# Optimization experiments

Measured on AMD Instinct MI355X. Metric: run time of the kernel, lower is better.

The kernel has to match this reference:

```python
import jax, jax.numpy as jnp
import numpy as np

N, E1, E2, P, H = 4096, 131072, 131072, 65536, 128
ROLE_VOCAB, ROLE_DIM, IDX_VOCAB, IDX_DIM = 8, 16, 1024, 8


def _lin_init(key, fan_in, fan_out):
    k1, k2 = jax.random.split(key)
    bound = 1.0 / np.sqrt(fan_in)
    W = jax.random.uniform(k1, (fan_in, fan_out), jnp.float32, -bound, bound)
    b = jax.random.uniform(k2, (fan_out,), jnp.float32, -bound, bound)
    return W, b


def setup_inputs() -> dict:
    key = jax.random.key(0)
    ks = jax.random.split(key, 24)
    d = {}
    d["block_features"] = jax.random.normal(ks[0], (N, 16), jnp.float32)
    d["role_ids"] = jax.random.randint(ks[1], (N,), 0, ROLE_VOCAB)
    d["b2b_src"] = jax.random.randint(ks[2], (E1,), 0, N)
    d["b2b_dst"] = jax.random.randint(ks[3], (E1,), 0, N)
    d["b2b_w"] = jax.random.uniform(ks[4], (E1,), jnp.float32)
    d["p2b_pin"] = jax.random.randint(ks[5], (E2,), 0, P)
    d["p2b_block"] = jax.random.randint(ks[6], (E2,), 0, N)
    d["p2b_w"] = jax.random.uniform(ks[7], (E2,), jnp.float32)
    d["pins_pos"] = jax.random.normal(ks[8], (P, 2), jnp.float32)
    d["area_targets"] = jax.random.uniform(ks[9], (N,), jnp.float32)
    # parameters
    d["role_emb"] = jax.random.normal(ks[10], (ROLE_VOCAB, ROLE_DIM), jnp.float32)
    d["idx_emb"] = jax.random.normal(ks[11], (IDX_VOCAB, IDX_DIM), jnp.float32)
    d["in_W1"], d["in_b1"] = _lin_init(ks[12], 16 + IDX_DIM + ROLE_DIM, H)
    d["in_W2"], d["in_b2"] = _lin_init(ks[13], H, H)
    d["b2b_W1"], d["b2b_b1"] = _lin_init(ks[14], 2 * H + 1, H)
    d["b2b_W2"], d["b2b_b2"] = _lin_init(ks[15], H, H)
    d["p2b_W1"], d["p2b_b1"] = _lin_init(ks[16], H + 3, H)
    d["p2b_W2"], d["p2b_b2"] = _lin_init(ks[17], H, H)
    d["self_W"], d["self_b"] = _lin_init(ks[18], H, H)
    d["ln_g"] = jnp.ones((H,), jnp.float32)
    d["ln_b"] = jnp.zeros((H,), jnp.float32)
    d["gp_W1"], d["gp_b1"] = _lin_init(ks[19], 2 * H, H)
    d["gp_W2"], d["gp_b2"] = _lin_init(ks[20], H, H)
    return d


def _mlp2(x, W1, b1, W2, b2):
    return jax.nn.relu(x @ W1 + b1) @ W2 + b2


def _forward(block_features, role_ids, b2b_src, b2b_dst, b2b_w, p2b_pin, p2b_block,
             p2b_w, pins_pos, area_targets, role_emb, idx_emb, in_W1, in_b1, in_W2,
             in_b2, b2b_W1, b2b_b1, b2b_W2, b2b_b2, p2b_W1, p2b_b1, p2b_W2, p2b_b2,
             self_W, self_b, ln_g, ln_b, gp_W1, gp_b1, gp_W2, gp_b2):
    n = block_features.shape[0]
    role_e = role_emb[role_ids]                       # [N, role_dim]
    idx_e = idx_emb[jnp.arange(n) % IDX_VOCAB]        # [N, idx_dim]
    x = jnp.concatenate([block_features, role_e, idx_e], axis=-1)
    h = jax.nn.relu(_mlp2(x, in_W1, in_b1, in_W2, in_b2))  # input_proj ends in ReLU

    # --- b2b messages: two directed messages per undirected edge ---
    max_b2b = jax.lax.stop_gradient(jnp.maximum(jnp.max(jnp.abs(b2b_w)), 1.0))
    w = (b2b_w / max_b2b)[:, None]                    # [E1, 1]
    hi, hj = h[b2b_src], h[b2b_dst]                   # [E1, H]
    m_ij = _mlp2(jnp.concatenate([hi, hj, w], -1), b2b_W1, b2b_b1, b2b_W2, b2b_b2)
    m_ji = _mlp2(jnp.concatenate([hj, hi, w], -1), b2b_W1, b2b_b1, b2b_W2, b2b_b2)
    agg = jnp.zeros_like(h).at[b2b_src].add(m_ij).at[b2b_dst].add(m_ji)

    # --- p2b messages ---
    total_area = jnp.maximum(jnp.sum(area_targets), 1e-6)
    case_scale = jax.lax.stop_gradient(jnp.maximum(jnp.sqrt(total_area), 1e-6))
    max_p2b = jax.lax.stop_gradient(jnp.maximum(jnp.max(jnp.abs(p2b_w)), 1.0))
    pin_feats = jnp.concatenate(
        [pins_pos[p2b_pin] / case_scale, (p2b_w / max_p2b)[:, None]], axis=-1)  # [E2, 3]
    m_p = _mlp2(jnp.concatenate([h[p2b_block], pin_feats], -1),
                p2b_W1, p2b_b1, p2b_W2, p2b_b2)
    agg = agg.at[p2b_block].add(m_p)

    # --- combine + LayerNorm ---
    z = h @ self_W + self_b + agg
    mu = jnp.mean(z, axis=-1, keepdims=True)
    var = jnp.mean(jnp.square(z - mu), axis=-1, keepdims=True)
    block_embeddings = (z - mu) / jnp.sqrt(var + 1e-5) * ln_g + ln_b

    pooled = jnp.concatenate(
        [block_embeddings.mean(axis=0), block_embeddings.max(axis=0)], axis=-1)
    graph_embedding = _mlp2(pooled, gp_W1, gp_b1, gp_W2, gp_b2)
    return block_embeddings, graph_embedding


def reference(block_features, role_ids, b2b_src, b2b_dst, b2b_w, p2b_pin, p2b_block,
              p2b_w, pins_pos, area_targets, role_emb, idx_emb, in_W1, in_b1, in_W2,
              in_b2, b2b_W1, b2b_b1, b2b_W2, b2b_b2, p2b_W1, p2b_b1, p2b_W2, p2b_b2,
              self_W, self_b, ln_g, ln_b, gp_W1, gp_b1, gp_W2, gp_b2):
    block_embeddings, graph_embedding = _forward(
        block_features, role_ids, b2b_src, b2b_dst, b2b_w, p2b_pin, p2b_block,
        p2b_w, pins_pos, area_targets, role_emb, idx_emb, in_W1, in_b1, in_W2,
        in_b2, b2b_W1, b2b_b1, b2b_W2, b2b_b2, p2b_W1, p2b_b1, p2b_W2, p2b_b2,
        self_W, self_b, ln_g, ln_b, gp_W1, gp_b1, gp_W2, gp_b2)
    block_mask = jnp.ones((block_features.shape[0],), dtype=bool)
    return block_embeddings, graph_embedding, block_mask
```

## Files before the change

### kernel.cpp

```cpp
#include <hip/hip_runtime.h>
#include <hip/hip_bf16.h>

#define N_NODES 4096
#define HDIM    128
#define E1      131072
#define E2      131072
#define NMSG_B2B (2 * E1)
#define CAPB    192
#define CAPP    96

#define OFF_PSUM   8
#define OFF_PMAX   136
#define OFF_HB     264
#define OFF_P      (OFF_HB + 262144)
#define OFF_Q      (OFF_P + 524288)
#define OFF_R      (OFF_Q + 524288)
#define OFF_CP     (OFF_R + 524288)
#define OFF_B2H    (OFF_CP + 24576)
#define OFF_B2L    (OFF_B2H + 8192)
#define OFF_P2H    (OFF_B2L + 8192)
#define OFF_P2L    (OFF_P2H + 8192)
#define OFF_SWP    (OFF_P2L + 8192)
#define OFF_IW1    (OFF_SWP + 8192)
#define OFF_IW2    (OFF_IW1 + 4096)
#define OFF_WLAST  (OFF_IW2 + 8192)
#define OFF_PEXTRA (OFF_WLAST + 128)
#define OFF_CNTB   (OFF_PEXTRA + 384)
#define OFF_CNTP   (OFF_CNTB + 4096)
#define OFF_BKB    (OFF_CNTP + 4096)
#define OFF_BKP    (OFF_BKB + 2 * N_NODES * CAPB)
#define WS_FLOATS  (OFF_BKP + 2 * N_NODES * CAPP)

typedef short short8 __attribute__((ext_vector_type(8)));
typedef float f32x4 __attribute__((ext_vector_type(4)));

__device__ __forceinline__ unsigned short f2bf(float f) {
  union { float f; unsigned u; } v; v.f = f;
  unsigned r = v.u + 0x7fffu + ((v.u >> 16) & 1u);
  return (unsigned short)(r >> 16);
}
__device__ __forceinline__ float bf2f(unsigned short h) {
  return __uint_as_float((unsigned)h << 16);
}
__device__ __forceinline__ int il(int c) { return ((c & 63) << 1) | (c >> 6); }

__global__ __launch_bounds__(256) void setup_kernel(const float* __restrict__ b2bw,
                                                    const float* __restrict__ p2bw,
                                                    const float* __restrict__ area,
                                                    const float* __restrict__ bW1,
                                                    const float* __restrict__ bW2,
                                                    const float* __restrict__ pW1,
                                                    const float* __restrict__ pW2,
                                                    const float* __restrict__ sWm,
                                                    const float* __restrict__ iW1,
                                                    const float* __restrict__ iW2,
                                                    float* __restrict__ ws) {
  __shared__ float red[256];
  int b = blockIdx.x, t = threadIdx.x;
  if (b < 32) {
    float m = 0.f;
    for (int i = b * 256 + t; i < E1; i += 32 * 256) m = fmaxf(m, fabsf(b2bw[i]));
    red[t] = m; __syncthreads();
    for (int s = 128; s > 0; s >>= 1) { if (t < s) red[t] = fmaxf(red[t], red[t + s]); __syncthreads(); }
    if (t == 0) atomicMax((unsigned*)&ws[0], __float_as_uint(red[0]));
  } else if (b < 64) {
    float m = 0.f;
    for (int i = (b - 32) * 256 + t; i < E2; i += 32 * 256) m = fmaxf(m, fabsf(p2bw[i]));
    red[t] = m; __syncthreads();
    for (int s = 128; s > 0; s >>= 1) { if (t < s) red[t] = fmaxf(red[t], red[t + s]); __syncthreads(); }
    if (t == 0) atomicMax((unsigned*)&ws[1], __float_as_uint(red[0]));
  } else if (b < 96) {
    float s0 = 0.f;
    for (int i = (b - 64) * 256 + t; i < N_NODES; i += 32 * 256) s0 += area[i];
    red[t] = s0; __syncthreads();
    for (int s = 128; s > 0; s >>= 1) { if (t < s) red[t] += red[t + s]; __syncthreads(); }
    if (t == 0) atomicAdd(&ws[2], red[0]);
  } else if (b == 96) {
    if (t < HDIM) ((int*)ws)[OFF_PMAX + t] = 0x80000000;
  } else {
    unsigned short* Cp  = (unsigned short*)(ws + OFF_CP);
    unsigned short* B2h = (unsigned short*)(ws + OFF_B2H);
    unsigned short* B2l = (unsigned short*)(ws + OFF_B2L);
    unsigned short* P2h = (unsigned short*)(ws + OFF_P2H);
    unsigned short* P2l = (unsigned short*)(ws + OFF_P2L);
    unsigned short* Swp = (unsigned short*)(ws + OFF_SWP);
    unsigned short* I1p = (unsigned short*)(ws + OFF_IW1);
    unsigned short* I2p = (unsigned short*)(ws + OFF_IW2);
    float* wlast = ws + OFF_WLAST;
    float* pextra = ws + OFF_PEXTRA;
    const int total = 156160;
    for (int x = (b - 97) * 256 + t; x < total; x += 128 * 256) {
      if (x < 49152) {
        int j = x & 7, lane = (x >> 3) & 63, ks = (x >> 9) & 3, nc = x >> 11;
        int col = nc * 16 + (lane & 15), k = ks * 32 + (lane >> 4) * 8 + j;
        float v;
        if (col < 128)      v = bW1[k * 128 + col];
        else if (col < 256) v = bW1[(128 + k) * 128 + (col - 128)];
        else                v = pW1[k * 128 + (col - 256)];
        Cp[x] = f2bf(v);
      } else if (x < 114688) {
        int u = (x - 49152) & 16383, which = (x - 49152) >> 14;
        int j = u & 7, lane = (u >> 3) & 63, ks = (u >> 9) & 3, nt = u >> 11;
        int n = nt * 16 + (lane & 15), k = ks * 32 + (lane >> 4) * 8 + j;
        float v = (which < 2) ? bW2[k * 128 + n] : pW2[k * 128 + n];
        unsigned short hi = f2bf(v);
        unsigned short outv = (which & 1) ? f2bf(v - bf2f(hi)) : hi;
        ((which < 2) ? ((which & 1) ? B2l : B2h) : ((which & 1) ? P2l : P2h))[u] = outv;
      } else if (x < 131072) {
        int u = x - 114688;
        int j = u & 7, lane = (u >> 3) & 63, ks = (u >> 9) & 3, nt = u >> 11;
        int n = nt * 16 + (lane & 15), k = ks * 32 + (lane >> 4) * 8 + j;
        Swp[u] = f2bf(sWm[k * 128 + n]);
      } else if (x < 139264) {
        int u = x - 131072;
        int j = u & 7, lane = (u >> 3) & 63, ks = (u >> 9) & 1, nt = u >> 10;
        int n = nt * 16 + (lane & 15), k = ks * 32 + (lane >> 4) * 8 + j;
        I1p[u] = (k < 40) ? f2bf(iW1[k * 128 + n]) : 0;
      } else if (x < 155648) {
        int u = x - 139264;
        int j = u & 7, lane = (u >> 3) & 63, ks = (u >> 9) & 3, nt = u >> 11;
        int n = nt * 16 + (lane & 15), k = ks * 32 + (lane >> 4) * 8 + j;
        I2p[u] = f2bf(iW2[k * 128 + n]);
      } else if (x < 155776) {
        int c = x - 155648;
        wlast[il(c)] = bW1[256 * 128 + c];
      } else {
        int u = x - 155776;
        int r = u >> 7, c = u & 127;
        pextra[r * 128 + il(c)] = pW1[(128 + r) * 128 + c];
      }
    }
  }
}

__global__ __launch_bounds__(512) void mid_kernel(const int* __restrict__ src,
                                                  const int* __restrict__ dst,
                                                  const int* __restrict__ pblk,
                                                  const int* __restrict__ ppin,
                                                  const float* __restrict__ bwv,
                                                  const float* __restrict__ pwv,
                                                  const float* __restrict__ pins,
                                                  const float* __restrict__ bfeat,
                                                  const int* __restrict__ rid,
                                                  const float* __restrict__ remb,
                                                  const float* __restrict__ iemb,
                                                  const float* __restrict__ ib1,
                                                  const float* __restrict__ ib2,
                                                  const float* __restrict__ bb1,
                                                  const float* __restrict__ pb1,
                                                  float* __restrict__ ws,
                                                  unsigned short* __restrict__ hb) {
  __shared__ __attribute__((aligned(16))) unsigned short xs[16 * 72];
  __shared__ __attribute__((aligned(16))) unsigned short h1s[16 * 136];
  __shared__ __attribute__((aligned(16))) unsigned short hs[16 * 136];
  int tid = threadIdx.x;
  if (blockIdx.x < 768) {
    int i = blockIdx.x * 512 + tid;
    int* cntB = (int*)ws + OFF_CNTB;
    int* cntP = (int*)ws + OFF_CNTP;
    uint2* BKB = (uint2*)((int*)ws + OFF_BKB);
    uint2* BKP = (uint2*)((int*)ws + OFF_BKP);
    if (i < NMSG_B2B) {
      int e = i >> 1, d = i & 1;
      int tg = d ? dst[e] : src[e];
      int o  = d ? src[e] : dst[e];
      int pos = atomicAdd(&cntB[tg], 1);
      if (pos < CAPB) {
        uint2 v; v.x = (unsigned)o; v.y = __float_as_uint(bwv[e]);
        BKB[tg * CAPB + pos] = v;
      }
    } else {
      int e = i - NMSG_B2B;
      int pin = ppin[e];
      int tg = pblk[e];
      int pos = atomicAdd(&cntP[tg], 1);
      if (pos < CAPP) {
        uint2 v;
        v.x = ((unsigned)f2bf(pins[pin * 2 + 1]) << 16) | (unsigned)f2bf(pins[pin * 2]);
        v.y = __float_as_uint(pwv[e]);
        BKP[tg * CAPP + pos] = v;
      }
    }
    return;
  }
  const unsigned short* I1p = (const unsigned short*)(ws + OFF_IW1);
  const unsigned short* I2p = (const unsigned short*)(ws + OFF_IW2);
  const unsigned short* Cp  = (const unsigned short*)(ws + OFF_CP);
  float* P = ws + OFF_P;
  float* Q = ws + OFF_Q;
  float* R = ws + OFF_R;
  int n0 = (blockIdx.x - 768) * 16;
  for (int idx = tid; idx < 1024; idx += 512) {
    int m = idx >> 6, c = idx & 63;
    int n = n0 + m;
    float v = 0.f;
    if (c < 16)      v = bfeat[n * 16 + c];
    else if (c < 32) v = remb[rid[n] * 16 + (c - 16)];
    else if (c < 40) v = iemb[(n & 1023) * 8 + (c - 32)];
    xs[m * 72 + c] = f2bf(v);
  }
  __syncthreads();
  int lane = tid & 63, wv = tid >> 6;
  int l15 = lane & 15, q = lane >> 4;
  f32x4 zero = {0.f, 0.f, 0.f, 0.f};
  f32x4 a1 = zero;
#pragma unroll
  for (int ks = 0; ks < 2; ks++) {
    short8 af = *(const short8*)(&xs[l15 * 72 + ks * 32 + q * 8]);
    short8 bfr = *(const short8*)(I1p + ((wv * 2 + ks) * 64 + lane) * 8);
    a1 = __builtin_amdgcn_mfma_f32_16x16x32_bf16(af, bfr, a1, 0, 0, 0);
  }
  {
    int n = wv * 16 + l15;
    float b = ib1[n];
#pragma unroll
    for (int r = 0; r < 4; r++)
      h1s[(q * 4 + r) * 136 + n] = f2bf(fmaxf(a1[r] + b, 0.f));
  }
  __syncthreads();
  f32x4 a2 = zero;
#pragma unroll
  for (int ks = 0; ks < 4; ks++) {
    short8 af = *(const short8*)(&h1s[l15 * 136 + ks * 32 + q * 8]);
    short8 bfr = *(const short8*)(I2p + ((wv * 4 + ks) * 64 + lane) * 8);
    a2 = __builtin_amdgcn_mfma_f32_16x16x32_bf16(af, bfr, a2, 0, 0, 0);
  }
  {
    int n = wv * 16 + l15;
    float b = ib2[n];
#pragma unroll
    for (int r = 0; r < 4; r++) {
      unsigned short hv = f2bf(fmaxf(a2[r] + b, 0.f));
      hs[(q * 4 + r) * 136 + n] = hv;
      hb[(n0 + q * 4 + r) * 128 + n] = hv;
    }
  }
  __syncthreads();
  f32x4 a3[3];
#pragma unroll
  for (int i = 0; i < 3; i++) a3[i] = zero;
#pragma unroll
  for (int ks = 0; ks < 4; ks++) {
    short8 af = *(const short8*)(&hs[l15 * 136 + ks * 32 + q * 8]);
#pragma unroll
    for (int j = 0; j < 3; j++) {
      short8 bfr = *(const short8*)(Cp + (((3 * wv + j) * 4 + ks) * 64 + lane) * 8);
      a3[j] = __builtin_amdgcn_mfma_f32_16x16x32_bf16(af, bfr, a3[j], 0, 0, 0);
    }
  }
#pragma unroll
  for (int j = 0; j < 3; j++) {
    int col = (3 * wv + j) * 16 + l15;
    int arr = col >> 7, cc = col & 127;
    float bias = (arr == 0) ? bb1[cc] : ((arr == 2) ? pb1[cc] : 0.f);
    float* dstp = (arr == 0) ? P : ((arr == 1) ? Q : R);
    int ic = il(cc);
#pragma unroll
    for (int r = 0; r < 4; r++)
      dstp[(n0 + q * 4 + r) * 128 + ic] = a3[j][r] + bias;
  }
}

__global__ __launch_bounds__(1024) void fused_kernel(const unsigned short* __restrict__ hb,
                                                     const float* __restrict__ sb,
                                                     const float* __restrict__ lng,
                                                     const float* __restrict__ lnb,
                                                     const float* __restrict__ bb2,
                                                     const float* __restrict__ pb2,
                                                     const float* __restrict__ gW1,
                                                     const float* __restrict__ gb1,
                                                     const float* __restrict__ gW2,
                                                     const float* __restrict__ gb2,
                                                     float* __restrict__ ws,
                                                     float* __restrict__ out) {
  __shared__ __attribute__((aligned(16))) unsigned short A[16 * 648];
  __shared__ float zp[2][16 * 128];
  __shared__ float zs[16 * 133];
  __shared__ float muS[16], rsg[16];
  __shared__ float partS[16][16], partQ[16][16];
  __shared__ float psumL[8][128];
  __shared__ int   pmaxL[8][128];
  __shared__ int   isLast;
  int tid = threadIdx.x;
  int n0 = blockIdx.x * 16;
  int lane = tid & 63, wv = tid >> 6;
  if (tid < 256) {
    int m = tid >> 4, o = (tid & 15) * 8;
    *(uint4*)(&A[m * 648 + o]) = *(const uint4*)(hb + (n0 + m) * 128 + o);
  }
  {
    const int* cntB = (const int*)ws + OFF_CNTB;
    const int* cntP = (const int*)ws + OFF_CNTP;
    const uint2* BKB = (const uint2*)((const int*)ws + OFF_BKB);
    const uint2* BKP = (const uint2*)((const int*)ws + OFF_BKP);
    const float* Pm = ws + OFF_P;
    const float* Qm = ws + OFF_Q;
    const float* Rm = ws + OFF_R;
    float invb = 1.f / fmaxf(__uint_as_float(((const unsigned*)ws)[0]), 1.f);
    float invp = 1.f / fmaxf(__uint_as_float(((const unsigned*)ws)[1]), 1.f);
    float cs = fmaxf(sqrtf(fmaxf(ws[2], 1e-6f)), 1e-6f);
    float invc = 1.f / cs;
    float2 wlr = *(const float2*)(ws + OFF_WLAST + 2 * lane);
    float2 e0r = *(const float2*)(ws + OFF_PEXTRA + 2 * lane);
    float2 e1r = *(const float2*)(ws + OFF_PEXTRA + 128 + 2 * lane);
    float2 e2r = *(const float2*)(ws + OFF_PEXTRA + 256 + 2 * lane);
    float2 wl = {invb * wlr.x, invb * wlr.y};
    float2 e0 = {invc * e0r.x, invc * e0r.y};
    float2 e1 = {invc * e1r.x, invc * e1r.y};
    float2 e2 = {invp * e2r.x, invp * e2r.y};
    int ln = wv;
    int node = n0 + ln;
    {
      int cnt = min(cntB[node], CAPB);
      const uint2* bk = BKB + node * CAPB;
      float2 p = *(const float2*)(Pm + node * 128 + 2 * lane);
      float a0 = 0.f, a1 = 0.f, b0 = 0.f, b1 = 0.f;
      int m = 0;
      for (; m + 8 <= cnt; m += 8) {
        uint2 k0 = bk[m],     k1 = bk[m + 1], k2 = bk[m + 2], k3 = bk[m + 3];
        uint2 k4 = bk[m + 4], k5 = bk[m + 5], k6 = bk[m + 6], k7 = bk[m + 7];
        float2 q0 = *(const float2*)(Qm + k0.x * 128 + 2 * lane);
        float2 q1 = *(const float2*)(Qm + k1.x * 128 + 2 * lane);
        float2 q2 = *(const float2*)(Qm + k2.x * 128 + 2 * lane);
        float2 q3 = *(const float2*)(Qm + k3.x * 128 + 2 * lane);
        float2 q4 = *(const float2*)(Qm + k4.x * 128 + 2 * lane);
        float2 q5 = *(const float2*)(Qm + k5.x * 128 + 2 * lane);
        float2 q6 = *(const float2*)(Qm + k6.x * 128 + 2 * lane);
        float2 q7 = *(const float2*)(Qm + k7.x * 128 + 2 * lane);
        float w0 = __uint_as_float(k0.y), w1 = __uint_as_float(k1.y);
        float w2 = __uint_as_float(k2.y), w3 = __uint_as_float(k3.y);
        float w4 = __uint_as_float(k4.y), w5 = __uint_as_float(k5.y);
        float w6 = __uint_as_float(k6.y), w7 = __uint_as_float(k7.y);
        a0 += fmaxf(fmaf(w0, wl.x, p.x) + q0.x, 0.f);
        a1 += fmaxf(fmaf(w0, wl.y, p.y) + q0.y, 0.f);
        b0 += fmaxf(fmaf(w1, wl.x, p.x) + q1.x, 0.f);
        b1 += fmaxf(fmaf(w1, wl.y, p.y) + q1.y, 0.f);
        a0 += fmaxf(fmaf(w2, wl.x, p.x) + q2.x, 0.f);
        a1 += fmaxf(fmaf(w2, wl.y, p.y) + q2.y, 0.f);
        b0 += fmaxf(fmaf(w3, wl.x, p.x) + q3.x, 0.f);
        b1 += fmaxf(fmaf(w3, wl.y, p.y) + q3.y, 0.f);
        a0 += fmaxf(fmaf(w4, wl.x, p.x) + q4.x, 0.f);
        a1 += fmaxf(fmaf(w4, wl.y, p.y) + q4.y, 0.f);
        b0 += fmaxf(fmaf(w5, wl.x, p.x) + q5.x, 0.f);
        b1 += fmaxf(fmaf(w5, wl.y, p.y) + q5.y, 0.f);
        a0 += fmaxf(fmaf(w6, wl.x, p.x) + q6.x, 0.f);
        a1 += fmaxf(fmaf(w6, wl.y, p.y) + q6.y, 0.f);
        b0 += fmaxf(fmaf(w7, wl.x, p.x) + q7.x, 0.f);
        b1 += fmaxf(fmaf(w7, wl.y, p.y) + q7.y, 0.f);
      }
      for (; m < cnt; m++) {
        uint2 k0 = bk[m];
        float w0 = __uint_as_float(k0.y);
        float2 q0 = *(const float2*)(Qm + k0.x * 128 + 2 * lane);
        a0 += fmaxf(fmaf(w0, wl.x, p.x) + q0.x, 0.f);
        a1 += fmaxf(fmaf(w0, wl.y, p.y) + q0.y, 0.f);
      }
      float s0 = a0 + b0;
      float s1 = a1 + b1;
      unsigned short h0 = f2bf(s0);
      A[ln * 648 + 128 + lane] = h0;
      A[ln * 648 + 256 + lane] = f2bf(s0 - bf2f(h0));
      unsigned short h1v = f2bf(s1);
      A[ln * 648 + 128 + 64 + lane] = h1v;
      A[ln * 648 + 256 + 64 + lane] = f2bf(s1 - bf2f(h1v));
    }
    {
      int cnt = min(cntP[node], CAPP);
      const uint2* bk = BKP + node * CAPP;
      float2 r = *(const float2*)(Rm + node * 128 + 2 * lane);
      float a0 = 0.f, a1 = 0.f, b0 = 0.f, b1 = 0.f;
      int m = 0;
      for (; m + 4 <= cnt; m += 4) {
        uint2 k0 = bk[m], k1 = bk[m + 1], k2 = bk[m + 2], k3 = bk[m + 3];
        float x00 = __uint_as_float((k0.x & 0xFFFFu) << 16);
        float x01 = __uint_as_float(k0.x & 0xFFFF0000u);
        float x02 = __uint_as_float(k0.y);
        float x10 = __uint_as_float((k1.x & 0xFFFFu) << 16);
        float x11 = __uint_as_float(k1.x & 0xFFFF0000u);
        float x12 = __uint_as_float(k1.y);
        float x20 = __uint_as_float((k2.x & 0xFFFFu) << 16);
        float x21 = __uint_as_float(k2.x & 0xFFFF0000u);
        float x22 = __uint_as_float(k2.y);
        float x30 = __uint_as_float((k3.x & 0xFFFFu) << 16);
        float x31 = __uint_as_float(k3.x & 0xFFFF0000u);
        float x32 = __uint_as_float(k3.y);
        a0 += fmaxf(fmaf(x02, e2.x, fmaf(x01, e1.x, fmaf(x00, e0.x, r.x))), 0.f);
        a1 += fmaxf(fmaf(x02, e2.y, fmaf(x01, e1.y, fmaf(x00, e0.y, r.y))), 0.f);
        b0 += fmaxf(fmaf(x12, e2.x, fmaf(x11, e1.x, fmaf(x10, e0.x, r.x))), 0.f);
        b1 += fmaxf(fmaf(x12, e2.y, fmaf(x11, e1.y, fmaf(x10, e0.y, r.y))), 0.f);
        a0 += fmaxf(fmaf(x22, e2.x, fmaf(x21, e1.x, fmaf(x20, e0.x, r.x))), 0.f);
        a1 += fmaxf(fmaf(x22, e2.y, fmaf(x21, e1.y, fmaf(x20, e0.y, r.y))), 0.f);
        b0 += fmaxf(fmaf(x32, e2.x, fmaf(x31, e1.x, fmaf(x30, e0.x, r.x))), 0.f);
        b1 += fmaxf(fmaf(x32, e2.y, fmaf(x31, e1.y, fmaf(x30, e0.y, r.y))), 0.f);
      }
      for (; m < cnt; m++) {
        uint2 k0 = bk[m];
        float x00 = __uint_as_float((k0.x & 0xFFFFu) << 16);
        float x01 = __uint_as_float(k0.x & 0xFFFF0000u);
        float x02 = __uint_as_float(k0.y);
        a0 += fmaxf(fmaf(x02, e2.x, fmaf(x01, e1.x, fmaf(x00, e0.x, r.x))), 0.f);
        a1 += fmaxf(fmaf(x02, e2.y, fmaf(x01, e1.y, fmaf(x00, e0.y, r.y))), 0.f);
      }
      float s0 = a0 + b0;
      float s1 = a1 + b1;
      unsigned short h0 = f2bf(s0);
      A[ln * 648 + 384 + lane] = h0;
      A[ln * 648 + 512 + lane] = f2bf(s0 - bf2f(h0));
      unsigned short h1v = f2bf(s1);
      A[ln * 648 + 384 + 64 + lane] = h1v;
      A[ln * 648 + 512 + 64 + lane] = f2bf(s1 - bf2f(h1v));
    }
  }
  __syncthreads();
  int l15 = lane & 15, q = lane >> 4;
  int ct = wv & 7, half = wv >> 3;
  f32x4 zero = {0.f, 0.f, 0.f, 0.f};
  f32x4 acc = zero;
  const unsigned short* bufs[7] = {
    (const unsigned short*)(ws + OFF_SWP), (const unsigned short*)(ws + OFF_B2H),
    (const unsigned short*)(ws + OFF_B2L), (const unsigned short*)(ws + OFF_B2H),
    (const unsigned short*)(ws + OFF_P2H), (const unsigned short*)(ws + OFF_P2L),
    (const unsigned short*)(ws + OFF_P2H)};
  const int segs[7] = {0, 128, 128, 256, 384, 384, 512};
  int p0 = half ? 4 : 0, p1 = half ? 7 : 4;
  for (int p = p0; p < p1; p++) {
#pragma unroll
    for (int ks = 0; ks < 4; ks++) {
      short8 af = *(const short8*)(&A[l15 * 648 + segs[p] + ks * 32 + q * 8]);
      short8 bfr = *(const short8*)(bufs[p] + ((ct * 4 + ks) * 64 + lane) * 8);
      acc = __builtin_amdgcn_mfma_f32_16x16x32_bf16(af, bfr, acc, 0, 0, 0);
    }
  }
  {
    int nn = ct * 16 + l15;
#pragma unroll
    for (int r = 0; r < 4; r++)
      zp[half][(q * 4 + r) * 128 + nn] = acc[r];
  }
  __syncthreads();
  const int* cntB = (const int*)ws + OFF_CNTB;
  const int* cntP = (const int*)ws + OFF_CNTP;
  {
    int idx = tid;
    for (int rep = 0; rep < 2; rep++, idx += 1024) {
      int row = idx >> 7, c = idx & 127;
      float cb = (float)cntB[n0 + row], cp = (float)cntP[n0 + row];
      zs[row * 133 + c] = zp[0][row * 128 + c] + zp[1][row * 128 + c]
                        + sb[c] + cb * bb2[c] + cp * pb2[c];
    }
  }
  __syncthreads();
  if (tid < 256) {
    int r = tid >> 4, g = tid & 15;
    const float* zr = &zs[r * 133 + g * 8];
    float s = 0.f, s2 = 0.f;
#pragma unroll
    for (int i = 0; i < 8; i++) { float v = zr[i]; s += v; s2 += v * v; }
    partS[r][g] = s; partQ[r][g] = s2;
  }
  __syncthreads();
  if (tid < 16) {
    float s = 0.f, s2 = 0.f;
#pragma unroll
    for (int g = 0; g < 16; g++) { s += partS[tid][g]; s2 += partQ[tid][g]; }
    float m = s * (1.f / 128.f);
    float var = s2 * (1.f / 128.f) - m * m;
    muS[tid] = m;
    rsg[tid] = rsqrtf(fmaxf(var, 0.f) + 1e-5f);
  }
  __syncthreads();
  {
    int c = tid & 127, grp = tid >> 7;
    float g = lng[c], b = lnb[c];
    float ls = 0.f; int lm = 0x80000000;
    for (int r = grp * 2; r < grp * 2 + 2; r++) {
      float v = (zs[r * 133 + c] - muS[r]) * rsg[r] * g + b;
      out[(n0 + r) * 128 + c] = v;
      ls += v;
      int e = __float_as_int(v);
      e = e >= 0 ? e : (e ^ 0x7fffffff);
      lm = max(lm, e);
    }
    psumL[grp][c] = ls; pmaxL[grp][c] = lm;
  }
  __syncthreads();
  if (tid < 128) {
    float s = 0.f; int mx = 0x80000000;
#pragma unroll
    for (int g = 0; g < 8; g++) { s += psumL[g][tid]; mx = max(mx, pmaxL[g][tid]); }
    atomicAdd(&ws[OFF_PSUM + tid], s);
    atomicMax(&((int*)ws)[OFF_PMAX + tid], mx);
  }
  if (tid < 16) out[N_NODES * HDIM + HDIM + n0 + tid] = 1.0f;
  __syncthreads();
  if (tid == 0) {
    __threadfence();
    int v = atomicAdd(&((int*)ws)[3], 1);
    isLast = (v == (int)gridDim.x - 1);
  }
  __syncthreads();
  if (!isLast) return;
  __shared__ float pooled[256];
  __shared__ float gpart[8][128];
  __shared__ float g1[128];
  if (tid < 128) {
    pooled[tid] = atomicAdd(&ws[OFF_PSUM + tid], 0.f) * (1.f / (float)N_NODES);
  } else if (tid < 256) {
    int e = atomicAdd(&((int*)ws)[OFF_PMAX + (tid - 128)], 0);
    int bits = e >= 0 ? e : (e ^ 0x7fffffff);
    pooled[tid] = __int_as_float(bits);
  }
  __syncthreads();
  {
    int c = tid & 127, g = tid >> 7;
    float acc2 = 0.f;
#pragma unroll 8
    for (int k = g * 32; k < g * 32 + 32; k++) acc2 += pooled[k] * gW1[k * 128 + c];
    gpart[g][c] = acc2;
  }
  __syncthreads();
  if (tid < 128) {
    float s = gb1[tid];
#pragma unroll
    for (int g = 0; g < 8; g++) s += gpart[g][tid];
    g1[tid] = fmaxf(s, 0.f);
  }
  __syncthreads();
  {
    int c = tid & 127, g = tid >> 7;
    float acc2 = 0.f;
#pragma unroll 8
    for (int k = g * 16; k < g * 16 + 16; k++) acc2 += g1[k] * gW2[k * 128 + c];
    gpart[g][c] = acc2;
  }
  __syncthreads();
  if (tid < 128) {
    float s = gb2[tid];
#pragma unroll
    for (int g = 0; g < 8; g++) s += gpart[g][tid];
    out[N_NODES * HDIM + tid] = s;
  }
}

extern "C" void kernel_launch(void* const* d_in, const int* in_sizes, int n_in,
                              void* d_out, int out_size, void* d_ws, size_t ws_size,
                              hipStream_t stream) {
  const float* bfeat = (const float*)d_in[0];
  const int*   rid   = (const int*)d_in[1];
  const int*   bsrc  = (const int*)d_in[2];
  const int*   bdst  = (const int*)d_in[3];
  const float* bw    = (const float*)d_in[4];
  const int*   ppin  = (const int*)d_in[5];
  const int*   pblk  = (const int*)d_in[6];
  const float* pw    = (const float*)d_in[7];
  const float* pins  = (const float*)d_in[8];
  const float* area  = (const float*)d_in[9];
  const float* remb  = (const float*)d_in[10];
  const float* iemb  = (const float*)d_in[11];
  const float* inW1  = (const float*)d_in[12];
  const float* inb1  = (const float*)d_in[13];
  const float* inW2  = (const float*)d_in[14];
  const float* inb2  = (const float*)d_in[15];
  const float* bW1   = (const float*)d_in[16];
  const float* bb1   = (const float*)d_in[17];
  const float* bW2   = (const float*)d_in[18];
  const float* bb2   = (const float*)d_in[19];
  const float* pW1   = (const float*)d_in[20];
  const float* pb1   = (const float*)d_in[21];
  const float* pW2   = (const float*)d_in[22];
  const float* pb2   = (const float*)d_in[23];
  const float* sW    = (const float*)d_in[24];
  const float* sb    = (const float*)d_in[25];
  const float* lng   = (const float*)d_in[26];
  const float* lnb   = (const float*)d_in[27];
  const float* gW1   = (const float*)d_in[28];
  const float* gb1   = (const float*)d_in[29];
  const float* gW2   = (const float*)d_in[30];
  const float* gb2   = (const float*)d_in[31];

  float* ws  = (float*)d_ws;
  float* out = (float*)d_out;
  unsigned short* hb = (unsigned short*)(ws + OFF_HB);
  int* cntB = (int*)ws + OFF_CNTB;

  hipMemsetAsync(d_ws, 0, 264 * sizeof(float), stream);
  hipMemsetAsync((void*)cntB, 0, 2 * 4096 * sizeof(int), stream);
  setup_kernel<<<225, 256, 0, stream>>>(bw, pw, area,
                                        bW1, bW2, pW1, pW2, sW, inW1, inW2, ws);
  mid_kernel<<<1024, 512, 0, stream>>>(bsrc, bdst, pblk, ppin, bw, pw, pins,
                                       bfeat, rid, remb, iemb, inb1, inb2, bb1, pb1,
                                       ws, hb);
  fused_kernel<<<256, 1024, 0, stream>>>(hb, sb, lng, lnb, bb2, pb2,
                                         gW1, gb1, gW2, gb2, ws, out);
}
```

Measured before the change: 195.6 us.

## Split wave into half-waves gathering float4 rows with prefetched bucket keys

The edge-aggregation loops in the fused kernel now have each half of a wave process alternate edges, with 32 lanes loading float4 slices of a 128-wide row instead of 64 lanes loading float2. The two halves are combined with a cross-half shuffle. The b2b loop software-prefetches the next group of bucket keys so index loads overlap the gathers. The count-buffer zeroing moves from a separate memset into setup_kernel, removing one launch, in exchange for extra shuffles and packed LDS stores.

After: 191.0 us. 1.02x faster.

```diff
diff --git a/kernel.cpp b/kernel.cpp
--- a/kernel.cpp
+++ b/kernel.cpp
@@ -43,6 +43,12 @@
   return __uint_as_float((unsigned)h << 16);
 }
 __device__ __forceinline__ int il(int c) { return ((c & 63) << 1) | (c >> 6); }
+__device__ __forceinline__ f32x4 relu4(f32x4 v) {
+  f32x4 r;
+  r[0] = fmaxf(v[0], 0.f); r[1] = fmaxf(v[1], 0.f);
+  r[2] = fmaxf(v[2], 0.f); r[3] = fmaxf(v[3], 0.f);
+  return r;
+}
 
 __global__ __launch_bounds__(256) void setup_kernel(const float* __restrict__ b2bw,
                                                     const float* __restrict__ p2bw,
@@ -77,6 +83,8 @@
     if (t == 0) atomicAdd(&ws[2], red[0]);
   } else if (b == 96) {
     if (t < HDIM) ((int*)ws)[OFF_PMAX + t] = 0x80000000;
+    int* cB = (int*)ws + OFF_CNTB;
+    for (int i = t; i < 2 * N_NODES; i += 256) cB[i] = 0;
   } else {
     unsigned short* Cp  = (unsigned short*)(ws + OFF_CP);
     unsigned short* B2h = (unsigned short*)(ws + OFF_B2H);
@@ -284,13 +292,13 @@
   int tid = threadIdx.x;
   int n0 = blockIdx.x * 16;
   int lane = tid & 63, wv = tid >> 6;
+  const int* cntBp = (const int*)ws + OFF_CNTB;
+  const int* cntPp = (const int*)ws + OFF_CNTP;
   if (tid < 256) {
     int m = tid >> 4, o = (tid & 15) * 8;
     *(uint4*)(&A[m * 648 + o]) = *(const uint4*)(hb + (n0 + m) * 128 + o);
   }
   {
-    const int* cntB = (const int*)ws + OFF_CNTB;
-    const int* cntP = (const int*)ws + OFF_CNTP;
     const uint2* BKB = (const uint2*)((const int*)ws + OFF_BKB);
     const uint2* BKP = (const uint2*)((const int*)ws + OFF_BKP);
     const float* Pm = ws + OFF_P;
@@ -300,115 +308,116 @@
     float invp = 1.f / fmaxf(__uint_as_float(((const unsigned*)ws)[1]), 1.f);
     float cs = fmaxf(sqrtf(fmaxf(ws[2], 1e-6f)), 1e-6f);
     float invc = 1.f / cs;
-    float2 wlr = *(const float2*)(ws + OFF_WLAST + 2 * lane);
-    float2 e0r = *(const float2*)(ws + OFF_PEXTRA + 2 * lane);
-    float2 e1r = *(const float2*)(ws + OFF_PEXTRA + 128 + 2 * lane);
-    float2 e2r = *(const float2*)(ws + OFF_PEXTRA + 256 + 2 * lane);
-    float2 wl = {invb * wlr.x, invb * wlr.y};
-    float2 e0 = {invc * e0r.x, invc * e0r.y};
-    float2 e1 = {invc * e1r.x, invc * e1r.y};
-    float2 e2 = {invp * e2r.x, invp * e2r.y};
+    int l5 = lane & 31, hf = lane >> 5;
+    f32x4 wl = *(const f32x4*)(ws + OFF_WLAST + 4 * l5);
+    f32x4 e0 = *(const f32x4*)(ws + OFF_PEXTRA + 4 * l5);
+    f32x4 e1 = *(const f32x4*)(ws + OFF_PEXTRA + 128 + 4 * l5);
+    f32x4 e2 = *(const f32x4*)(ws + OFF_PEXTRA + 256 + 4 * l5);
+    wl *= invb; e0 *= invc; e1 *= invc; e2 *= invp;
     int ln = wv;
     int node = n0 + ln;
     {
-      int cnt = min(cntB[node], CAPB);
+      int cnt = min(cntBp[node], CAPB);
       const uint2* bk = BKB + node * CAPB;
-      float2 p = *(const float2*)(Pm + node * 128 + 2 * lane);
-      float a0 = 0.f, a1 = 0.f, b0 = 0.f, b1 = 0.f;
+      f32x4 p4 = *(const f32x4*)(Pm + node * 128 + 4 * l5);
+      f32x4 acc = {0.f, 0.f, 0.f, 0.f};
       int m = 0;
-      for (; m + 8 <= cnt; m += 8) {
-        uint2 k0 = bk[m],     k1 = bk[m + 1], k2 = bk[m + 2], k3 = bk[m + 3];
-        uint2 k4 = bk[m + 4], k5 = bk[m + 5], k6 = bk[m + 6], k7 = bk[m + 7];
-        float2 q0 = *(const float2*)(Qm + k0.x * 128 + 2 * lane);
-        float2 q1 = *(const float2*)(Qm + k1.x * 128 + 2 * lane);
-        float2 q2 = *(const float2*)(Qm + k2.x * 128 + 2 * lane);
-        float2 q3 = *(const float2*)(Qm + k3.x * 128 + 2 * lane);
-        float2 q4 = *(const float2*)(Qm + k4.x * 128 + 2 * lane);
-        float2 q5 = *(const float2*)(Qm + k5.x * 128 + 2 * lane);
-        float2 q6 = *(const float2*)(Qm + k6.x * 128 + 2 * lane);
-        float2 q7 = *(const float2*)(Qm + k7.x * 128 + 2 * lane);
-        float w0 = __uint_as_float(k0.y), w1 = __uint_as_float(k1.y);
-        float w2 = __uint_as_float(k2.y), w3 = __uint_as_float(k3.y);
-        float w4 = __uint_as_float(k4.y), w5 = __uint_as_float(k5.y);
-        float w6 = __uint_as_float(k6.y), w7 = __uint_as_float(k7.y);
-        a0 += fmaxf(fmaf(w0, wl.x, p.x) + q0.x, 0.f);
-        a1 += fmaxf(fmaf(w0, wl.y, p.y) + q0.y, 0.f);
-        b0 += fmaxf(fmaf(w1, wl.x, p.x) + q1.x, 0.f);
-        b1 += fmaxf(fmaf(w1, wl.y, p.y) + q1.y, 0.f);
-        a0 += fmaxf(fmaf(w2, wl.x, p.x) + q2.x, 0.f);
-        a1 += fmaxf(fmaf(w2, wl.y, p.y) + q2.y, 0.f);
-        b0 += fmaxf(fmaf(w3, wl.x, p.x) + q3.x, 0.f);
-        b1 += fmaxf(fmaf(w3, wl.y, p.y) + q3.y, 0.f);
-        a0 += fmaxf(fmaf(w4, wl.x, p.x) + q4.x, 0.f);
-        a1 += fmaxf(fmaf(w4, wl.y, p.y) + q4.y, 0.f);
-        b0 += fmaxf(fmaf(w5, wl.x, p.x) + q5.x, 0.f);
-        b1 += fmaxf(fmaf(w5, wl.y, p.y) + q5.y, 0.f);
-        a0 += fmaxf(fmaf(w6, wl.x, p.x) + q6.x, 0.f);
-        a1 += fmaxf(fmaf(w6, wl.y, p.y) + q6.y, 0.f);
-        b0 += fmaxf(fmaf(w7, wl.x, p.x) + q7.x, 0.f);
-        b1 += fmaxf(fmaf(w7, wl.y, p.y) + q7.y, 0.f);
-      }
-      for (; m < cnt; m++) {
-        uint2 k0 = bk[m];
-        float w0 = __uint_as_float(k0.y);
-        float2 q0 = *(const float2*)(Qm + k0.x * 128 + 2 * lane);
-        a0 += fmaxf(fmaf(w0, wl.x, p.x) + q0.x, 0.f);
-        a1 += fmaxf(fmaf(w0, wl.y, p.y) + q0.y, 0.f);
-      }
-      float s0 = a0 + b0;
-      float s1 = a1 + b1;
-      unsigned short h0 = f2bf(s0);
-      A[ln * 648 + 128 + lane] = h0;
-      A[ln * 648 + 256 + lane] = f2bf(s0 - bf2f(h0));
-      unsigned short h1v = f2bf(s1);
-      A[ln * 648 + 128 + 64 + lane] = h1v;
-      A[ln * 648 + 256 + 64 + lane] = f2bf(s1 - bf2f(h1v));
+      if (cnt >= 8) {
+        uint2 k0 = bk[hf], k1 = bk[2 + hf], k2 = bk[4 + hf], k3 = bk[6 + hf];
+        while (m + 16 <= cnt) {
+          uint2 t0 = bk[m + 8 + hf],  t1 = bk[m + 10 + hf];
+          uint2 t2 = bk[m + 12 + hf], t3 = bk[m + 14 + hf];
+          f32x4 q0 = *(const f32x4*)(Qm + k0.x * 128 + 4 * l5);
+          f32x4 q1 = *(const f32x4*)(Qm + k1.x * 128 + 4 * l5);
+          f32x4 q2 = *(const f32x4*)(Qm + k2.x * 128 + 4 * l5);
+          f32x4 q3 = *(const f32x4*)(Qm + k3.x * 128 + 4 * l5);
+          acc += relu4(p4 + __uint_as_float(k0.y) * wl + q0);
+          acc += relu4(p4 + __uint_as_float(k1.y) * wl + q1);
+          acc += relu4(p4 + __uint_as_float(k2.y) * wl + q2);
+          acc += relu4(p4 + __uint_as_float(k3.y) * wl + q3);
+          k0 = t0; k1 = t1; k2 = t2; k3 = t3;
+          m += 8;
+        }
+        f32x4 q0 = *(const f32x4*)(Qm + k0.x * 128 + 4 * l5);
+        f32x4 q1 = *(const f32x4*)(Qm + k1.x * 128 + 4 * l5);
+        f32x4 q2 = *(const f32x4*)(Qm + k2.x * 128 + 4 * l5);
+        f32x4 q3 = *(const f32x4*)(Qm + k3.x * 128 + 4 * l5);
+        acc += relu4(p4 + __uint_as_float(k0.y) * wl + q0);
+        acc += relu4(p4 + __uint_as_float(k1.y) * wl + q1);
+        acc += relu4(p4 + __uint_as_float(k2.y) * wl + q2);
+        acc += relu4(p4 + __uint_as_float(k3.y) * wl + q3);
+        m += 8;
+      }
+      for (; m + 2 <= cnt; m += 2) {
+        uint2 k = bk[m + hf];
+        f32x4 q = *(const f32x4*)(Qm + k.x * 128 + 4 * l5);
+        acc += relu4(p4 + __uint_as_float(k.y) * wl + q);
+      }
+      if (m < cnt) {
+        uint2 k = bk[m + hf];
+        f32x4 q = *(const f32x4*)(Qm + (k.x & (N_NODES - 1)) * 128 + 4 * l5);
+        f32x4 v = relu4(p4 + __uint_as_float(k.y) * wl + q);
+        if (hf == 0) acc += v;
+      }
+      f32x4 tot;
+#pragma unroll
+      for (int j = 0; j < 4; j++) tot[j] = acc[j] + __shfl_xor(acc[j], 32, 64);
+      if (hf == 0) {
+        unsigned short h0 = f2bf(tot[0]), h1 = f2bf(tot[1]);
+        unsigned short h2 = f2bf(tot[2]), h3 = f2bf(tot[3]);
+        *(unsigned*)(&A[ln * 648 + 128 + 2 * l5])      = (unsigned)h0 | ((unsigned)h2 << 16);
+        *(unsigned*)(&A[ln * 648 + 128 + 64 + 2 * l5]) = (unsigned)h1 | ((unsigned)h3 << 16);
+        unsigned short g0 = f2bf(tot[0] - bf2f(h0)), g1 = f2bf(tot[1] - bf2f(h1));
+        unsigned short g2 = f2bf(tot[2] - bf2f(h2)), g3 = f2bf(tot[3] - bf2f(h3));
+        *(unsigned*)(&A[ln * 648 + 256 + 2 * l5])      = (unsigned)g0 | ((unsigned)g2 << 16);
+        *(unsigned*)(&A[ln * 648 + 256 + 64 + 2 * l5]) = (unsigned)g1 | ((unsigned)g3 << 16);
+      }
     }
     {
-      int cnt = min(cntP[node], CAPP);
+      int cnt = min(cntPp[node], CAPP);
       const uint2* bk = BKP + node * CAPP;
-      float2 r = *(const float2*)(Rm + node * 128 + 2 * lane);
-      float a0 = 0.f, a1 = 0.f, b0 = 0.f, b1 = 0.f;
+      f32x4 r4 = *(const f32x4*)(Rm + node * 128 + 4 * l5);
+      f32x4 acc = {0.f, 0.f, 0.f, 0.f};
       int m = 0;
       for (; m + 4 <= cnt; m += 4) {
-        uint2 k0 = bk[m], k1 = bk[m + 1], k2 = bk[m + 2], k3 = bk[m + 3];
-        float x00 = __uint_as_float((k0.x & 0xFFFFu) << 16);
-        float x01 = __uint_as_float(k0.x & 0xFFFF0000u);
-        float x02 = __uint_as_float(k0.y);
-        float x10 = __uint_as_float((k1.x & 0xFFFFu) << 16);
-        float x11 = __uint_as_float(k1.x & 0xFFFF0000u);
-        float x12 = __uint_as_float(k1.y);
-        float x20 = __uint_as_float((k2.x & 0xFFFFu) << 16);
-        float x21 = __uint_as_float(k2.x & 0xFFFF0000u);
-        float x22 = __uint_as_float(k2.y);
-        float x30 = __uint_as_float((k3.x & 0xFFFFu) << 16);
-        float x31 = __uint_as_float(k3.x & 0xFFFF0000u);
-        float x32 = __uint_as_float(k3.y);
-        a0 += fmaxf(fmaf(x02, e2.x, fmaf(x01, e1.x, fmaf(x00, e0.x, r.x))), 0.f);
-        a1 += fmaxf(fmaf(x02, e2.y, fmaf(x01, e1.y, fmaf(x00, e0.y, r.y))), 0.f);
-        b0 += fmaxf(fmaf(x12, e2.x, fmaf(x11, e1.x, fmaf(x10, e0.x, r.x))), 0.f);
-        b1 += fmaxf(fmaf(x12, e2.y, fmaf(x11, e1.y, fmaf(x10, e0.y, r.y))), 0.f);
-        a0 += fmaxf(fmaf(x22, e2.x, fmaf(x21, e1.x, fmaf(x20, e0.x, r.x))), 0.f);
-        a1 += fmaxf(fmaf(x22, e2.y, fmaf(x21, e1.y, fmaf(x20, e0.y, r.y))), 0.f);
-        b0 += fmaxf(fmaf(x32, e2.x, fmaf(x31, e1.x, fmaf(x30, e0.x, r.x))), 0.f);
-        b1 += fmaxf(fmaf(x32, e2.y, fmaf(x31, e1.y, fmaf(x30, e0.y, r.y))), 0.f);
-      }
-      for (; m < cnt; m++) {
-        uint2 k0 = bk[m];
-        float x00 = __uint_as_float((k0.x & 0xFFFFu) << 16);
-        float x01 = __uint_as_float(k0.x & 0xFFFF0000u);
-        float x02 = __uint_as_float(k0.y);
-        a0 += fmaxf(fmaf(x02, e2.x, fmaf(x01, e1.x, fmaf(x00, e0.x, r.x))), 0.f);
-        a1 += fmaxf(fmaf(x02, e2.y, fmaf(x01, e1.y, fmaf(x00, e0.y, r.y))), 0.f);
-      }
-      float s0 = a0 + b0;
-      float s1 = a1 + b1;
-      unsigned short h0 = f2bf(s0);
-      A[ln * 648 + 384 + lane] = h0;
-      A[ln * 648 + 512 + lane] = f2bf(s0 - bf2f(h0));
-      unsigned short h1v = f2bf(s1);
-      A[ln * 648 + 384 + 64 + lane] = h1v;
-      A[ln * 648 + 512 + 64 + lane] = f2bf(s1 - bf2f(h1v));
+        uint2 ka = bk[m + hf], kb = bk[m + 2 + hf];
+        float a0 = __uint_as_float((ka.x & 0xFFFFu) << 16);
+        float a1 = __uint_as_float(ka.x & 0xFFFF0000u);
+        float a2 = __uint_as_float(ka.y);
+        float b0 = __uint_as_float((kb.x & 0xFFFFu) << 16);
+        float b1 = __uint_as_float(kb.x & 0xFFFF0000u);
+        float b2 = __uint_as_float(kb.y);
+        acc += relu4(r4 + a0 * e0 + a1 * e1 + a2 * e2);
+        acc += relu4(r4 + b0 * e0 + b1 * e1 + b2 * e2);
+      }
+      for (; m + 2 <= cnt; m += 2) {
+        uint2 ka = bk[m + hf];
+        float a0 = __uint_as_float((ka.x & 0xFFFFu) << 16);
+        float a1 = __uint_as_float(ka.x & 0xFFFF0000u);
+        float a2 = __uint_as_float(ka.y);
+        acc += relu4(r4 + a0 * e0 + a1 * e1 + a2 * e2);
+      }
+      if (m < cnt) {
+        uint2 ka = bk[m + hf];
+        float a0 = __uint_as_float((ka.x & 0xFFFFu) << 16);
+        float a1 = __uint_as_float(ka.x & 0xFFFF0000u);
+        float a2 = __uint_as_float(ka.y);
+        f32x4 v = relu4(r4 + a0 * e0 + a1 * e1 + a2 * e2);
+        if (hf == 0) acc += v;
+      }
+      f32x4 tot;
+#pragma unroll
+      for (int j = 0; j < 4; j++) tot[j] = acc[j] + __shfl_xor(acc[j], 32, 64);
+      if (hf == 0) {
+        unsigned short h0 = f2bf(tot[0]), h1 = f2bf(tot[1]);
+        unsigned short h2 = f2bf(tot[2]), h3 = f2bf(tot[3]);
+        *(unsigned*)(&A[ln * 648 + 384 + 2 * l5])      = (unsigned)h0 | ((unsigned)h2 << 16);
+        *(unsigned*)(&A[ln * 648 + 384 + 64 + 2 * l5]) = (unsigned)h1 | ((unsigned)h3 << 16);
+        unsigned short g0 = f2bf(tot[0] - bf2f(h0)), g1 = f2bf(tot[1] - bf2f(h1));
+        unsigned short g2 = f2bf(tot[2] - bf2f(h2)), g3 = f2bf(tot[3] - bf2f(h3));
+        *(unsigned*)(&A[ln * 648 + 512 + 2 * l5])      = (unsigned)g0 | ((unsigned)g2 << 16);
+        *(unsigned*)(&A[ln * 648 + 512 + 64 + 2 * l5]) = (unsigned)g1 | ((unsigned)g3 << 16);
+      }
     }
   }
   __syncthreads();
@@ -438,13 +447,11 @@
       zp[half][(q * 4 + r) * 128 + nn] = acc[r];
   }
   __syncthreads();
-  const int* cntB = (const int*)ws + OFF_CNTB;
-  const int* cntP = (const int*)ws + OFF_CNTP;
   {
     int idx = tid;
     for (int rep = 0; rep < 2; rep++, idx += 1024) {
       int row = idx >> 7, c = idx & 127;
-      float cb = (float)cntB[n0 + row], cp = (float)cntP[n0 + row];
+      float cb = (float)cntBp[n0 + row], cp = (float)cntPp[n0 + row];
       zs[row * 133 + c] = zp[0][row * 128 + c] + zp[1][row * 128 + c]
                         + sb[c] + cb * bb2[c] + cp * pb2[c];
     }
@@ -581,10 +588,8 @@
   float* ws  = (float*)d_ws;
   float* out = (float*)d_out;
   unsigned short* hb = (unsigned short*)(ws + OFF_HB);
-  int* cntB = (int*)ws + OFF_CNTB;
 
   hipMemsetAsync(d_ws, 0, 264 * sizeof(float), stream);
-  hipMemsetAsync((void*)cntB, 0, 2 * 4096 * sizeof(int), stream);
   setup_kernel<<<225, 256, 0, stream>>>(bw, pw, area,
                                         bW1, bW2, pW1, pW2, sW, inW1, inW2, ws);
   mid_kernel<<<1024, 512, 0, stream>>>(bsrc, bdst, pblk, ppin, bw, pw, pins,
```
